# Optimization experiments

Measured on AMD Instinct MI355X. Metric: run time of the kernel, lower is better.

Reference implementation:

```python
import jax, jax.numpy as jnp
import numpy as np
from jax import lax

DIM = 128
K = 3
PAD = K // 2


def setup_inputs() -> dict:
    key = jax.random.key(0)
    k1, k2, k3, k4, k5 = jax.random.split(key, 5)
    B, H, W = 64, 32, 32
    wdim = DIM * DIM * K * K + DIM  # 147584
    # scale question_rep (it encodes conv weights) for numerical sanity
    question_rep = jax.random.normal(k1, (B, wdim), dtype=jnp.float32) * 0.05
    lhs_rep = jax.random.normal(k2, (B, DIM, H, W), dtype=jnp.float32)
    rhs_rep = jax.random.normal(k3, (B, DIM, H, W), dtype=jnp.float32)
    proj_w = jax.random.normal(k4, (DIM, 2 * DIM), dtype=jnp.float32) * (1.0 / np.sqrt(2 * DIM))
    proj_b = jax.random.normal(k5, (DIM,), dtype=jnp.float32) * 0.01
    return {"question_rep": question_rep, "lhs_rep": lhs_rep,
            "rhs_rep": rhs_rep, "proj_w": proj_w, "proj_b": proj_b}


def _per_sample_conv(x, w, b):
    # x: [dim, H, W], w: [dim, dim, K, K], b: [dim]
    y = lax.conv_general_dilated(
        x[None], w, window_strides=(1, 1),
        padding=[(PAD, PAD), (PAD, PAD)],
        dimension_numbers=("NCHW", "OIHW", "NCHW"))
    return y[0] + b[:, None, None]


def reference(question_rep, lhs_rep, rhs_rep, proj_w, proj_b):
    B = question_rep.shape[0]
    wdim = DIM * DIM * K * K
    cnn_weight = question_rep[:, :wdim].reshape(B, DIM, DIM, K, K)
    cnn_bias = question_rep[:, wdim:]  # [B, dim]
    # 1x1 projection conv: cat along channels then contract
    cat = jnp.concatenate([lhs_rep, rhs_rep], axis=1)  # [B, 2*dim, H, W]
    cnn_inp = jnp.einsum("bchw,oc->bohw", cat, proj_w) + proj_b[None, :, None, None]
    # per-sample dynamic conv, vectorized over batch (equiv. grouped conv)
    out = jax.vmap(_per_sample_conv)(cnn_inp, cnn_weight, cnn_bias)
    return out
```

## Files before the change

kernel.cpp:

```cpp
#include <hip/hip_runtime.h>
#include <hip/hip_bf16.h>

#define QSTRIDE 147584
#define WOFF    147456

typedef __attribute__((ext_vector_type(8))) short bf16x8;
typedef __attribute__((ext_vector_type(4))) float f32x4;

static __device__ __forceinline__ ushort f2bf(float f) {
  union { float f; unsigned u; } x; x.f = f;
  unsigned r = x.u + 0x7fffu + ((x.u >> 16) & 1u);
  return (ushort)(r >> 16);
}
static __device__ __forceinline__ unsigned pk2(ushort a, ushort b) {
  return (unsigned)a | ((unsigned)b << 16);
}
static __device__ __forceinline__ void async16(const ushort* g, ushort* l) {
  __builtin_amdgcn_global_load_lds((const __attribute__((address_space(1))) void*)g,
                                   (__attribute__((address_space(3))) void*)l, 16, 0, 0);
}

__global__ __launch_bounds__(256) void pack_w_kernel(const float* __restrict__ q,
                                                     ushort* __restrict__ wt2) {
  int b = blockIdx.x >> 4, og = blockIdx.x & 15;
  int t = threadIdx.x;
  int o_loc = t >> 5, cq = (t >> 3) & 3, q4 = t & 7;
  int o_full = og * 8 + o_loc;
  int ci = cq * 32 + q4 * 4;
  const float4* src = (const float4*)(q + (size_t)b * QSTRIDE
                                        + (size_t)o_full * 1152 + (size_t)ci * 9);
  float4 ff[9];
#pragma unroll
  for (int i = 0; i < 9; ++i) ff[i] = src[i];
  const float* v = (const float*)ff;
  ushort* dd = wt2 + (size_t)b * 147456 + (size_t)cq * 4096 + o_full * 32 + q4 * 4;
#pragma unroll
  for (int tap = 0; tap < 9; ++tap) {
    uint2 pkv;
    pkv.x = pk2(f2bf(v[tap]),      f2bf(v[9 + tap]));
    pkv.y = pk2(f2bf(v[18 + tap]), f2bf(v[27 + tap]));
    *(uint2*)(dd + (size_t)tap * 16384) = pkv;
  }
}

__global__ __launch_bounds__(256) void pack_pw_kernel(const float* __restrict__ pw,
                                                      ushort* __restrict__ pwb2) {
  int tg = blockIdx.x * 256 + threadIdx.x;
  int o  = tg >> 5;
  int c0 = (tg & 31) * 8;
  const float4* s4 = (const float4*)(pw + (size_t)o * 256 + c0);
  float4 f0 = s4[0], f1 = s4[1];
  uint4 pkv;
  pkv.x = pk2(f2bf(f0.x), f2bf(f0.y)); pkv.y = pk2(f2bf(f0.z), f2bf(f0.w));
  pkv.z = pk2(f2bf(f1.x), f2bf(f1.y)); pkv.w = pk2(f2bf(f1.z), f2bf(f1.w));
  *(uint4*)(pwb2 + (size_t)(c0 >> 5) * 4096 + o * 32 + (c0 & 31)) = pkv;
}

__global__ __launch_bounds__(256) void zero_border_kernel(ushort* __restrict__ xp2) {
  int b = blockIdx.x, t = threadIdx.x;
  for (int idx = t; idx < 528; idx += 256) {
    int cq = idx / 132, r = idx - cq * 132;
    int hp, wp;
    if (r < 34)       { hp = 0;        wp = r; }
    else if (r < 68)  { hp = 33;       wp = r - 34; }
    else if (r < 100) { hp = r - 67;   wp = 0; }
    else              { hp = r - 99;   wp = 33; }
    uint4 z = {0u,0u,0u,0u};
    uint4* dst = (uint4*)(xp2 + (((size_t)b * 4 + cq) * 1156 + hp * 34 + wp) * 32);
#pragma unroll
    for (int i = 0; i < 4; ++i) dst[i] = z;
  }
}

__global__ __launch_bounds__(256, 4) void proj_kernel(const ushort* __restrict__ pwb2,
                                                      const float* __restrict__ lhs,
                                                      const float* __restrict__ rhs,
                                                      const float* __restrict__ pb,
                                                      ushort* __restrict__ xp2) {
  int b = blockIdx.y, p0 = blockIdx.x * 64;
  int t = threadIdx.x;
  int lane = t & 63, wv = t >> 6;
  int quad = lane >> 4, li = lane & 15;
  int px = p0 + wv * 16 + li;
  f32x4 acc[8] = {};
  const float* bl = lhs + (size_t)b * 131072 + (size_t)quad * 8192 + px;
  const float* br = rhs + (size_t)b * 131072 + (size_t)quad * 8192 + px;

#pragma unroll
  for (int c = 0; c < 8; ++c) {
    const float* s = (c < 4 ? bl : br) + (size_t)(c & 3) * 32768;
    float f[8];
#pragma unroll
    for (int j = 0; j < 8; ++j) f[j] = s[(size_t)j * 1024];
    union { uint4 u; bf16x8 v; } bu;
    bu.u.x = pk2(f2bf(f[0]), f2bf(f[1]));
    bu.u.y = pk2(f2bf(f[2]), f2bf(f[3]));
    bu.u.z = pk2(f2bf(f[4]), f2bf(f[5]));
    bu.u.w = pk2(f2bf(f[6]), f2bf(f[7]));
    bf16x8 bg = bu.v;
    const ushort* ap = pwb2 + (size_t)c * 4096 + li * 32 + quad * 8;
#pragma unroll
    for (int mi = 0; mi < 8; ++mi) {
      bf16x8 af = *(const bf16x8*)(ap + mi * 512);
      acc[mi] = __builtin_amdgcn_mfma_f32_16x16x32_bf16(af, bg, acc[mi], 0, 0, 0);
    }
  }

  ushort* xpb = xp2 + (size_t)b * 4 * 1156 * 32;
  int h = px >> 5, w = px & 31;
#pragma unroll
  for (int mi = 0; mi < 8; ++mi) {
    int o0 = mi * 16 + quad * 4;
    float4 bias = *(const float4*)(pb + o0);
    f32x4 a = acc[mi];
    uint2 pkv;
    pkv.x = pk2(f2bf(a.x + bias.x), f2bf(a.y + bias.y));
    pkv.y = pk2(f2bf(a.z + bias.z), f2bf(a.w + bias.w));
    ushort* dp = xpb + ((size_t)(o0 >> 5) * 1156 + (h + 1) * 34 + (w + 1)) * 32 + (o0 & 31);
    *(uint2*)dp = pkv;
  }
}

__global__ __launch_bounds__(256, 2) void conv_kernel(const ushort* __restrict__ wt2,
                                                      const ushort* __restrict__ xp2,
                                                      const float* __restrict__ q,
                                                      float* __restrict__ out) {
  __shared__ ushort Bs[2][6528];
  int blk = blockIdx.x;
  int b = blk & 63, tile = blk >> 6;
  int p0 = tile * 128, h0 = tile * 4;
  int t = threadIdx.x;
  int lane = t & 63, wv = t >> 6;
  int m0 = (wv & 1) * 64, n0 = (wv >> 1) * 64;
  int quad = lane >> 4, li = lane & 15;
  f32x4 acc[4][4] = {};
  const ushort* wtb = wt2 + (size_t)b * 147456;
  const ushort* xpb = xp2 + (size_t)b * 147968;

  auto stageB = [&](int cqi, int buf) {
    const ushort* bgp = xpb + (size_t)(cqi * 1156 + h0 * 34) * 32;
    int lb = wv * 204;
    async16(bgp + (size_t)(lb +       lane) * 8, &Bs[buf][0] + (lb      ) * 8);
    async16(bgp + (size_t)(lb +  64 + lane) * 8, &Bs[buf][0] + (lb +  64) * 8);
    async16(bgp + (size_t)(lb + 128 + lane) * 8, &Bs[buf][0] + (lb + 128) * 8);
    if (lane < 12)
      async16(bgp + (size_t)(lb + 192 + lane) * 8, &Bs[buf][0] + (lb + 192) * 8);
  };

  stageB(0, 0);

#pragma unroll
  for (int cq = 0; cq < 4; ++cq) {
    __syncthreads();
    if (cq < 3) stageB(cq + 1, (cq + 1) & 1);
    const ushort* bsr = &Bs[cq & 1][0];
    const ushort* wcq = wtb + (size_t)cq * 4096;
#pragma unroll
    for (int tap = 0; tap < 9; ++tap) {
      const ushort* ar = wcq + (size_t)tap * 16384;
      int kh = tap / 3, kw = tap - kh * 3;
      bf16x8 af[4], bg[4];
#pragma unroll
      for (int mi = 0; mi < 4; ++mi)
        af[mi] = *(const bf16x8*)(ar + (m0 + mi*16 + li) * 32 + quad * 8);
#pragma unroll
      for (int ni = 0; ni < 4; ++ni) {
        int pl = n0 + ni*16 + li;
        int hh = pl >> 5, ww = pl & 31;
        bg[ni] = *(const bf16x8*)(bsr + ((hh + kh) * 34 + (ww + kw)) * 32 + quad * 8);
      }
#pragma unroll
      for (int mi = 0; mi < 4; ++mi)
#pragma unroll
        for (int ni = 0; ni < 4; ++ni)
          acc[mi][ni] = __builtin_amdgcn_mfma_f32_16x16x32_bf16(af[mi], bg[ni], acc[mi][ni], 0, 0, 0);
    }
  }

  const float* qb = q + (size_t)b * QSTRIDE + WOFF;
  float* ob = out + (size_t)b * 128 * 1024 + p0;
#pragma unroll
  for (int mi = 0; mi < 4; ++mi) {
    int o0 = m0 + mi*16 + quad*4;
    float4 bias = *(const float4*)(qb + o0);
#pragma unroll
    for (int ni = 0; ni < 4; ++ni) {
      int pl = n0 + ni*16 + li;
      float* dp = ob + (size_t)o0 * 1024 + pl;
      f32x4 a = acc[mi][ni];
      dp[0]    = a.x + bias.x;
      dp[1024] = a.y + bias.y;
      dp[2048] = a.z + bias.z;
      dp[3072] = a.w + bias.w;
    }
  }
}

extern "C" void kernel_launch(void* const* d_in, const int* in_sizes, int n_in,
                              void* d_out, int out_size, void* d_ws, size_t ws_size,
                              hipStream_t stream) {
  const float* q   = (const float*)d_in[0];
  const float* lhs = (const float*)d_in[1];
  const float* rhs = (const float*)d_in[2];
  const float* pw  = (const float*)d_in[3];
  const float* pb  = (const float*)d_in[4];
  float* out = (float*)d_out;

  char* ws = (char*)d_ws;
  ushort* wt2  = (ushort*)(ws);
  ushort* pwb2 = (ushort*)(ws + 18874368);
  ushort* xp2  = (ushort*)(ws + 18939904);

  pack_w_kernel     <<<1024, 256, 0, stream>>>(q, wt2);
  pack_pw_kernel    <<<16,   256, 0, stream>>>(pw, pwb2);
  zero_border_kernel<<<64,   256, 0, stream>>>(xp2);
  proj_kernel       <<<dim3(16, 64), 256, 0, stream>>>(pwb2, lhs, rhs, pb, xp2);
  conv_kernel       <<<512,  256, 0, stream>>>(wt2, xp2, q, out);
}
```

Before: 193.9 us.

## Fuse projection into conv kernel with halo recompute; stage weight packing through LDS

The 1x1 projection is now computed inside the conv kernel for each 4-row tile plus a one-row halo, and written straight to LDS as bf16 with zeroed borders. This removes the separate proj and zero-border kernels and the global round trip of the padded intermediate. The cost is recomputing 1.5x the projection rows and losing the async double-buffered staging. Weight packing now goes through coalesced LDS loads with half as many blocks.

```diff
diff --git a/kernel.cpp b/kernel.cpp
--- a/kernel.cpp
+++ b/kernel.cpp
@@ -15,31 +15,34 @@
 static __device__ __forceinline__ unsigned pk2(ushort a, ushort b) {
   return (unsigned)a | ((unsigned)b << 16);
 }
-static __device__ __forceinline__ void async16(const ushort* g, ushort* l) {
-  __builtin_amdgcn_global_load_lds((const __attribute__((address_space(1))) void*)g,
-                                   (__attribute__((address_space(3))) void*)l, 16, 0, 0);
-}
 
 __global__ __launch_bounds__(256) void pack_w_kernel(const float* __restrict__ q,
                                                      ushort* __restrict__ wt2) {
-  int b = blockIdx.x >> 4, og = blockIdx.x & 15;
+  __shared__ float Ls[4608];
+  int b = blockIdx.x >> 3, ogrp = blockIdx.x & 7;
   int t = threadIdx.x;
-  int o_loc = t >> 5, cq = (t >> 3) & 3, q4 = t & 7;
-  int o_full = og * 8 + o_loc;
-  int ci = cq * 32 + q4 * 4;
-  const float4* src = (const float4*)(q + (size_t)b * QSTRIDE
-                                        + (size_t)o_full * 1152 + (size_t)ci * 9);
-  float4 ff[9];
-#pragma unroll
-  for (int i = 0; i < 9; ++i) ff[i] = src[i];
-  const float* v = (const float*)ff;
-  ushort* dd = wt2 + (size_t)b * 147456 + (size_t)cq * 4096 + o_full * 32 + q4 * 4;
-#pragma unroll
-  for (int tap = 0; tap < 9; ++tap) {
-    uint2 pkv;
-    pkv.x = pk2(f2bf(v[tap]),      f2bf(v[9 + tap]));
-    pkv.y = pk2(f2bf(v[18 + tap]), f2bf(v[27 + tap]));
-    *(uint2*)(dd + (size_t)tap * 16384) = pkv;
+  const float* gbase = q + (size_t)b * QSTRIDE + (size_t)ogrp * 16 * 1152;
+  ushort* dstb = wt2 + (size_t)b * 147456;
+  int o_loc = t >> 6;
+  int ci    = (t & 63) * 2;
+  int cq    = ci >> 5, coff = ci & 31;
+  for (int r = 0; r < 4; ++r) {
+    __syncthreads();
+    const float* gs = gbase + r * 4608;
+#pragma unroll
+    for (int i = 0; i < 18; ++i) Ls[i * 256 + t] = gs[i * 256 + t];
+    __syncthreads();
+    int o_full = ogrp * 16 + r * 4 + o_loc;
+    const float* v = Ls + o_loc * 1152 + ci * 9;
+    float a[18];
+#pragma unroll
+    for (int i = 0; i < 18; ++i) a[i] = v[i];
+    ushort* dd = dstb + (size_t)cq * 4096 + o_full * 32 + coff;
+#pragma unroll
+    for (int tap = 0; tap < 9; ++tap) {
+      unsigned pkv = pk2(f2bf(a[tap]), f2bf(a[9 + tap]));
+      *(unsigned*)(dd + (size_t)tap * 16384) = pkv;
+    }
   }
 }
 
@@ -56,104 +59,95 @@
   *(uint4*)(pwb2 + (size_t)(c0 >> 5) * 4096 + o * 32 + (c0 & 31)) = pkv;
 }
 
-__global__ __launch_bounds__(256) void zero_border_kernel(ushort* __restrict__ xp2) {
-  int b = blockIdx.x, t = threadIdx.x;
-  for (int idx = t; idx < 528; idx += 256) {
-    int cq = idx / 132, r = idx - cq * 132;
-    int hp, wp;
-    if (r < 34)       { hp = 0;        wp = r; }
-    else if (r < 68)  { hp = 33;       wp = r - 34; }
-    else if (r < 100) { hp = r - 67;   wp = 0; }
-    else              { hp = r - 99;   wp = 33; }
-    uint4 z = {0u,0u,0u,0u};
-    uint4* dst = (uint4*)(xp2 + (((size_t)b * 4 + cq) * 1156 + hp * 34 + wp) * 32);
-#pragma unroll
-    for (int i = 0; i < 4; ++i) dst[i] = z;
-  }
-}
-
-__global__ __launch_bounds__(256, 4) void proj_kernel(const ushort* __restrict__ pwb2,
-                                                      const float* __restrict__ lhs,
-                                                      const float* __restrict__ rhs,
-                                                      const float* __restrict__ pb,
-                                                      ushort* __restrict__ xp2) {
-  int b = blockIdx.y, p0 = blockIdx.x * 64;
-  int t = threadIdx.x;
-  int lane = t & 63, wv = t >> 6;
-  int quad = lane >> 4, li = lane & 15;
-  int px = p0 + wv * 16 + li;
-  f32x4 acc[8] = {};
-  const float* bl = lhs + (size_t)b * 131072 + (size_t)quad * 8192 + px;
-  const float* br = rhs + (size_t)b * 131072 + (size_t)quad * 8192 + px;
-
-#pragma unroll
-  for (int c = 0; c < 8; ++c) {
-    const float* s = (c < 4 ? bl : br) + (size_t)(c & 3) * 32768;
-    float f[8];
-#pragma unroll
-    for (int j = 0; j < 8; ++j) f[j] = s[(size_t)j * 1024];
-    union { uint4 u; bf16x8 v; } bu;
-    bu.u.x = pk2(f2bf(f[0]), f2bf(f[1]));
-    bu.u.y = pk2(f2bf(f[2]), f2bf(f[3]));
-    bu.u.z = pk2(f2bf(f[4]), f2bf(f[5]));
-    bu.u.w = pk2(f2bf(f[6]), f2bf(f[7]));
-    bf16x8 bg = bu.v;
-    const ushort* ap = pwb2 + (size_t)c * 4096 + li * 32 + quad * 8;
-#pragma unroll
-    for (int mi = 0; mi < 8; ++mi) {
-      bf16x8 af = *(const bf16x8*)(ap + mi * 512);
-      acc[mi] = __builtin_amdgcn_mfma_f32_16x16x32_bf16(af, bg, acc[mi], 0, 0, 0);
-    }
-  }
-
-  ushort* xpb = xp2 + (size_t)b * 4 * 1156 * 32;
-  int h = px >> 5, w = px & 31;
-#pragma unroll
-  for (int mi = 0; mi < 8; ++mi) {
-    int o0 = mi * 16 + quad * 4;
-    float4 bias = *(const float4*)(pb + o0);
-    f32x4 a = acc[mi];
-    uint2 pkv;
-    pkv.x = pk2(f2bf(a.x + bias.x), f2bf(a.y + bias.y));
-    pkv.y = pk2(f2bf(a.z + bias.z), f2bf(a.w + bias.w));
-    ushort* dp = xpb + ((size_t)(o0 >> 5) * 1156 + (h + 1) * 34 + (w + 1)) * 32 + (o0 & 31);
-    *(uint2*)dp = pkv;
-  }
-}
-
-__global__ __launch_bounds__(256, 2) void conv_kernel(const ushort* __restrict__ wt2,
-                                                      const ushort* __restrict__ xp2,
-                                                      const float* __restrict__ q,
-                                                      float* __restrict__ out) {
-  __shared__ ushort Bs[2][6528];
+__global__ __launch_bounds__(256, 2) void fused_conv_kernel(const ushort* __restrict__ wt2,
+                                                            const ushort* __restrict__ pwb2,
+                                                            const float* __restrict__ lhs,
+                                                            const float* __restrict__ rhs,
+                                                            const float* __restrict__ pb,
+                                                            const float* __restrict__ q,
+                                                            float* __restrict__ out) {
+  __shared__ ushort Bs[4][6][34][32];
   int blk = blockIdx.x;
   int b = blk & 63, tile = blk >> 6;
   int p0 = tile * 128, h0 = tile * 4;
   int t = threadIdx.x;
   int lane = t & 63, wv = t >> 6;
+  int quad = lane >> 4, li = lane & 15;
+
+  if (t < 48) {
+    int cq = t & 3, side = (t >> 2) & 1, rr = t >> 3;
+    uint4* z4 = (uint4*)&Bs[cq][rr][side ? 33 : 0][0];
+    uint4 z; z.x = z.y = z.z = z.w = 0u;
+    z4[0] = z; z4[1] = z; z4[2] = z; z4[3] = z;
+  }
+
+  {
+    int rk[3], wk[3], hk[3]; bool lv[3];
+#pragma unroll
+    for (int k = 0; k < 3; ++k) {
+      int nt = wv * 3 + k;
+      rk[k] = nt >> 1;
+      wk[k] = (nt & 1) * 16;
+      hk[k] = h0 - 1 + rk[k];
+      lv[k] = (hk[k] >= 0) && (hk[k] < 32);
+    }
+    f32x4 acc[3][8] = {};
+#pragma unroll
+    for (int c = 0; c < 8; ++c) {
+      const float* basep = (c < 4 ? lhs : rhs) + (size_t)b * 131072
+                         + (size_t)((c & 3) * 32 + quad * 8) * 1024;
+      bf16x8 bg[3];
+#pragma unroll
+      for (int k = 0; k < 3; ++k) {
+        union { uint4 u; bf16x8 v; } bu;
+        if (lv[k]) {
+          const float* s = basep + hk[k] * 32 + wk[k] + li;
+          float f[8];
+#pragma unroll
+          for (int j = 0; j < 8; ++j) f[j] = s[(size_t)j * 1024];
+          bu.u.x = pk2(f2bf(f[0]), f2bf(f[1]));
+          bu.u.y = pk2(f2bf(f[2]), f2bf(f[3]));
+          bu.u.z = pk2(f2bf(f[4]), f2bf(f[5]));
+          bu.u.w = pk2(f2bf(f[6]), f2bf(f[7]));
+        } else {
+          bu.u.x = bu.u.y = bu.u.z = bu.u.w = 0u;
+        }
+        bg[k] = bu.v;
+      }
+      const ushort* ap = pwb2 + (size_t)c * 4096 + li * 32 + quad * 8;
+#pragma unroll
+      for (int mi = 0; mi < 8; ++mi) {
+        bf16x8 af = *(const bf16x8*)(ap + mi * 512);
+#pragma unroll
+        for (int k = 0; k < 3; ++k)
+          acc[k][mi] = __builtin_amdgcn_mfma_f32_16x16x32_bf16(af, bg[k], acc[k][mi], 0, 0, 0);
+      }
+    }
+#pragma unroll
+    for (int k = 0; k < 3; ++k) {
+#pragma unroll
+      for (int mi = 0; mi < 8; ++mi) {
+        int o0 = mi * 16 + quad * 4;
+        uint2 pkv;
+        if (lv[k]) {
+          float4 bias = *(const float4*)(pb + o0);
+          f32x4 a = acc[k][mi];
+          pkv.x = pk2(f2bf(a.x + bias.x), f2bf(a.y + bias.y));
+          pkv.y = pk2(f2bf(a.z + bias.z), f2bf(a.w + bias.w));
+        } else {
+          pkv.x = 0u; pkv.y = 0u;
+        }
+        *(uint2*)&Bs[o0 >> 5][rk[k]][wk[k] + li + 1][o0 & 31] = pkv;
+      }
+    }
+  }
+  __syncthreads();
+
   int m0 = (wv & 1) * 64, n0 = (wv >> 1) * 64;
-  int quad = lane >> 4, li = lane & 15;
-  f32x4 acc[4][4] = {};
+  f32x4 acc2[4][4] = {};
   const ushort* wtb = wt2 + (size_t)b * 147456;
-  const ushort* xpb = xp2 + (size_t)b * 147968;
-
-  auto stageB = [&](int cqi, int buf) {
-    const ushort* bgp = xpb + (size_t)(cqi * 1156 + h0 * 34) * 32;
-    int lb = wv * 204;
-    async16(bgp + (size_t)(lb +       lane) * 8, &Bs[buf][0] + (lb      ) * 8);
-    async16(bgp + (size_t)(lb +  64 + lane) * 8, &Bs[buf][0] + (lb +  64) * 8);
-    async16(bgp + (size_t)(lb + 128 + lane) * 8, &Bs[buf][0] + (lb + 128) * 8);
-    if (lane < 12)
-      async16(bgp + (size_t)(lb + 192 + lane) * 8, &Bs[buf][0] + (lb + 192) * 8);
-  };
-
-  stageB(0, 0);
-
 #pragma unroll
   for (int cq = 0; cq < 4; ++cq) {
-    __syncthreads();
-    if (cq < 3) stageB(cq + 1, (cq + 1) & 1);
-    const ushort* bsr = &Bs[cq & 1][0];
     const ushort* wcq = wtb + (size_t)cq * 4096;
 #pragma unroll
     for (int tap = 0; tap < 9; ++tap) {
@@ -167,13 +161,13 @@
       for (int ni = 0; ni < 4; ++ni) {
         int pl = n0 + ni*16 + li;
         int hh = pl >> 5, ww = pl & 31;
-        bg[ni] = *(const bf16x8*)(bsr + ((hh + kh) * 34 + (ww + kw)) * 32 + quad * 8);
+        bg[ni] = *(const bf16x8*)&Bs[cq][hh + kh][ww + kw][quad * 8];
       }
 #pragma unroll
       for (int mi = 0; mi < 4; ++mi)
 #pragma unroll
         for (int ni = 0; ni < 4; ++ni)
-          acc[mi][ni] = __builtin_amdgcn_mfma_f32_16x16x32_bf16(af[mi], bg[ni], acc[mi][ni], 0, 0, 0);
+          acc2[mi][ni] = __builtin_amdgcn_mfma_f32_16x16x32_bf16(af[mi], bg[ni], acc2[mi][ni], 0, 0, 0);
     }
   }
 
@@ -187,7 +181,7 @@
     for (int ni = 0; ni < 4; ++ni) {
       int pl = n0 + ni*16 + li;
       float* dp = ob + (size_t)o0 * 1024 + pl;
-      f32x4 a = acc[mi][ni];
+      f32x4 a = acc2[mi][ni];
       dp[0]    = a.x + bias.x;
       dp[1024] = a.y + bias.y;
       dp[2048] = a.z + bias.z;
@@ -209,11 +203,8 @@
   char* ws = (char*)d_ws;
   ushort* wt2  = (ushort*)(ws);
   ushort* pwb2 = (ushort*)(ws + 18874368);
-  ushort* xp2  = (ushort*)(ws + 18939904);
-
-  pack_w_kernel     <<<1024, 256, 0, stream>>>(q, wt2);
-  pack_pw_kernel    <<<16,   256, 0, stream>>>(pw, pwb2);
-  zero_border_kernel<<<64,   256, 0, stream>>>(xp2);
-  proj_kernel       <<<dim3(16, 64), 256, 0, stream>>>(pwb2, lhs, rhs, pb, xp2);
-  conv_kernel       <<<512,  256, 0, stream>>>(wt2, xp2, q, out);
-}
+
+  pack_w_kernel    <<<512, 256, 0, stream>>>(q, wt2);
+  pack_pw_kernel   <<<16,  256, 0, stream>>>(pw, pwb2);
+  fused_conv_kernel<<<512, 256, 0, stream>>>(wt2, pwb2, lhs, rhs, pb, q, out);
+}
```

Result: faster. 181.4 us (-6.4%).
